# Performance work log

Measured on AMD Instinct MI355X. Metric: run time of the kernel, lower is better.

The kernel has to match this reference:

```python
import jax, jax.numpy as jnp
import numpy as np
from jax import lax


def setup_inputs() -> dict:
    key = jax.random.key(0)
    k1, k2, k3 = jax.random.split(key, 3)
    T, C, H, W = 8, 1024, 64, 64
    features = jax.random.normal(k1, (T, C, H, W), dtype=jnp.float32)
    # Single shared depthwise kernel ([Conv3d]*input_dim shares one module/weight)
    dw_weight = jax.random.normal(k2, (1, 1, 3, 3, 3), dtype=jnp.float32)
    # Pointwise 1x1x1 conv weight [out_c, in_c, 1, 1, 1]
    pw_weight = jax.random.normal(k3, (1024, 1024, 1, 1, 1), dtype=jnp.float32) * 0.03
    return {"features": features, "dw_weight": dw_weight, "pw_weight": pw_weight}


def reference(features, dw_weight, pw_weight):
    T, C, H, W = features.shape
    # torch: expand to [1,T,C,H,W] then torch.reshape to [1,C,T,H,W]
    # (a raw row-major reshape, NOT a transpose) -- replicate exactly.
    x = features.reshape(1, C, T, H, W)
    # Depthwise temporal conv: every channel uses the SAME [1,1,3,3,3] kernel
    # (the torch list is the same Conv3d object repeated). Express as one
    # grouped conv with the kernel tiled over channels.
    w_dw = jnp.tile(dw_weight, (C, 1, 1, 1, 1))  # [C,1,3,3,3]
    y = lax.conv_general_dilated(
        x, w_dw,
        window_strides=(1, 1, 1),
        padding=((1, 1), (1, 1), (1, 1)),
        feature_group_count=C,
        dimension_numbers=("NCDHW", "OIDHW", "NCDHW"),
    )  # [1,C,T,H,W]
    # Pointwise 1x1x1 conv: [C,C] channel-mixing GEMM per voxel.
    z = jnp.einsum("oc,bcthw->bothw", pw_weight[:, :, 0, 0, 0], y)
    # torch: reshape back [1,C,T,H,W] -> [1,T,C,H,W], then squeeze batch dim.
    return z.reshape(1, T, C, H, W)[0]
```

## Files before the change

kernel.cpp:

```cpp
#include <hip/hip_runtime.h>
#include <hip/hip_bf16.h>
#include <stdint.h>

typedef __attribute__((ext_vector_type(8))) short s8v;
typedef __attribute__((ext_vector_type(4))) float f4v;

#define T_TOT 8
#define NSP 32768
#define K_TOT 1024
#define M_TOT 1024

__device__ __forceinline__ unsigned short f2bf(float f) {
  unsigned int u = __float_as_uint(f);
  u += 0x7FFF + ((u >> 16) & 1);
  return (unsigned short)(u >> 16);
}

__global__ __launch_bounds__(256) void dw_kernel(const float* __restrict__ X,
                                                 const float* __restrict__ DW,
                                                 unsigned short* __restrict__ Yn,
                                                 const float* __restrict__ Wf,
                                                 unsigned short* __restrict__ Wb) {
  if (blockIdx.x == 4) {
    const int i = (blockIdx.y * 256 + threadIdx.x) * 4;
    float4 v = *(const float4*)&Wf[i];
    ushort4 o;
    o.x = f2bf(v.x); o.y = f2bf(v.y); o.z = f2bf(v.z); o.w = f2bf(v.w);
    *(ushort4*)&Wb[i] = o;
    return;
  }

  __shared__ float xin[8 * 18 * 64];
  const int tid = threadIdx.x;
  const int hb  = blockIdx.x;
  const int c   = blockIdx.y;
  const int h0  = hb * 16;

  float kw[27];
#pragma unroll
  for (int j = 0; j < 27; ++j) kw[j] = DW[j];

  const float* Xc = X + (size_t)c * NSP;

#pragma unroll
  for (int i = 0; i < 9; ++i) {
    const int f  = tid + i * 256;
    const int r  = f >> 4;
    const int wq = (f & 15) * 4;
    const int t  = r / 18;
    const int hr = r - t * 18;
    const int hg = h0 - 1 + hr;
    const int hc = min(max(hg, 0), 63);
    float4 v = *(const float4*)(Xc + (t * 64 + hc) * 64 + wq);
    if (hg != hc) v = (float4){0.f, 0.f, 0.f, 0.f};
    *(float4*)&xin[r * 64 + wq] = v;
  }
  __syncthreads();

  const int w  = tid & 63;
  const int hq = tid >> 6;
  const int wl = (w == 0)  ? w : w - 1;
  const int wr = (w == 63) ? w : w + 1;
  const float* bC = &xin[(hq * 4) * 64 + w];
  const float* bL = &xin[(hq * 4) * 64 + wl];
  const float* bR = &xin[(hq * 4) * 64 + wr];
  unsigned short* Yb = Yn + (size_t)c * NSP + (h0 + hq * 4) * 64 + w;

  float a0[4], a1[4], a2[4];
#pragma unroll
  for (int j = 0; j < 4; ++j) { a0[j] = 0.f; a1[j] = 0.f; a2[j] = 0.f; }

#pragma unroll
  for (int tp = 0; tp < 8; ++tp) {
    float v[6][3];
#pragma unroll
    for (int rr = 0; rr < 6; ++rr) {
      const int off = (tp * 18 + rr) * 64;
      float xc = bC[off];
      float xl = bL[off];
      float xr = bR[off];
      if (w == 0)  xl = 0.f;
      if (w == 63) xr = 0.f;
      v[rr][0] = xl; v[rr][1] = xc; v[rr][2] = xr;
    }
#pragma unroll
    for (int j = 0; j < 4; ++j)
#pragma unroll
      for (int kh = 0; kh < 3; ++kh)
#pragma unroll
        for (int kd = 0; kd < 3; ++kd) {
          const float xv = v[j + kh][kd];
          if (tp >= 1) a0[j] += kw[(2 * 3 + kh) * 3 + kd] * xv;
          a1[j] += kw[(1 * 3 + kh) * 3 + kd] * xv;
          if (tp <= 6) a2[j] += kw[(0 * 3 + kh) * 3 + kd] * xv;
        }
    if (tp >= 1) {
      unsigned short* yp = Yb + (size_t)(tp - 1) * 4096;
#pragma unroll
      for (int j = 0; j < 4; ++j) yp[j * 64] = f2bf(a0[j]);
    }
#pragma unroll
    for (int j = 0; j < 4; ++j) { a0[j] = a1[j]; a1[j] = a2[j]; a2[j] = 0.f; }
  }
  {
    unsigned short* yp = Yb + (size_t)7 * 4096;
#pragma unroll
    for (int j = 0; j < 4; ++j) yp[j * 64] = f2bf(a0[j]);
  }
}

__global__ __launch_bounds__(256) void tr_kernel(const unsigned short* __restrict__ Yn,
                                                 unsigned short* __restrict__ Yt) {
  __shared__ unsigned short tb[64][68];
  const int tid = threadIdx.x;
  const int n0  = blockIdx.x * 64;
  const int c0  = blockIdx.y * 64;

#pragma unroll
  for (int i = 0; i < 2; ++i) {
    const int cl = (tid >> 3) + i * 32;
    const int n8 = (tid & 7) * 8;
    const uint4 v = *(const uint4*)(Yn + (size_t)(c0 + cl) * NSP + n0 + n8);
    uint2 lo; lo.x = v.x; lo.y = v.y;
    uint2 hi; hi.x = v.z; hi.y = v.w;
    *(uint2*)&tb[cl][n8]     = lo;
    *(uint2*)&tb[cl][n8 + 4] = hi;
  }
  __syncthreads();

  const int nl = tid >> 2;
  const int cq = tid & 3;
#pragma unroll
  for (int i = 0; i < 2; ++i) {
    const int c8 = cq * 8 + i * 32;
    unsigned int p[4];
#pragma unroll
    for (int j = 0; j < 4; ++j) {
      const unsigned int a = tb[c8 + 2 * j][nl];
      const unsigned int b = tb[c8 + 2 * j + 1][nl];
      p[j] = a | (b << 16);
    }
    uint4 o; o.x = p[0]; o.y = p[1]; o.z = p[2]; o.w = p[3];
    *(uint4*)(Yt + (size_t)(n0 + nl) * 1024 + c0 + c8) = o;
  }
}

__device__ __forceinline__ void gload_lds16(const void* g, void* lds) {
  __builtin_amdgcn_global_load_lds(
      (const __attribute__((address_space(1))) void*)(uintptr_t)g,
      (__attribute__((address_space(3))) void*)(uintptr_t)lds, 16, 0, 0);
}

__global__ __launch_bounds__(512, 2) void gemm8_kernel(const unsigned short* __restrict__ A,
                                                       const unsigned short* __restrict__ B,
                                                       float* __restrict__ C) {
  __shared__ char smem[131072];
  const int tid  = threadIdx.x;
  const int lane = tid & 63;
  const int wid  = tid >> 6;
  const int wm   = wid >> 2, wn = wid & 3;

  const int wg = (int)blockIdx.x;
  const int lg = (wg & 7) * 64 + (wg >> 3);
  const int bm = lg & 3;
  const int bn = lg >> 2;

  f4v acc[8][4];
#pragma unroll
  for (int i = 0; i < 8; ++i)
#pragma unroll
    for (int j = 0; j < 4; ++j) acc[i][j] = (f4v){0.f, 0.f, 0.f, 0.f};

  const int r  = tid >> 2;
  const int kb = (((tid & 3) ^ ((tid >> 3) & 3)) * 8);
  const unsigned short* ga = A + (size_t)(bm * 256 + r) * K_TOT + kb;
  const unsigned short* gb = B + (size_t)(bn * 256 + r) * K_TOT + kb;
  const int stg = wid * 1024;

#define STAGE_KK(nb, tt, kk)                                                  \
  do {                                                                        \
    const int ko = (tt) * 64 + (kk) * 32;                                     \
    char* ab = smem + (nb) + (kk) * 16384 + stg;                              \
    char* bb = smem + (nb) + 32768 + (kk) * 16384 + stg;                      \
    gload_lds16(ga + ko,                 ab);                                 \
    gload_lds16(ga + 128 * K_TOT + ko,   ab + 8192);                          \
    gload_lds16(gb + ko,                 bb);                                 \
    gload_lds16(gb + 128 * K_TOT + ko,   bb + 8192);                          \
  } while (0)

  const int cph  = ((lane >> 4) ^ ((lane >> 1) & 3)) * 8;
  const int arow = wm * 128 + (lane & 15);
  const int brow = wn * 64  + (lane & 15);

#define PHASE(cu, nx, tt, kk, pf)                                             \
  do {                                                                        \
    const unsigned short* Ac = (const unsigned short*)(smem + (cu));          \
    const unsigned short* Bc = (const unsigned short*)(smem + (cu) + 32768);  \
    s8v av[8], bv[4];                                                         \
    _Pragma("unroll")                                                         \
    for (int nf = 0; nf < 4; ++nf)                                            \
      bv[nf] = *(const s8v*)&Bc[(kk) * 8192 + (brow + nf * 16) * 32 + cph];   \
    _Pragma("unroll")                                                         \
    for (int mf = 0; mf < 8; ++mf)                                            \
      av[mf] = *(const s8v*)&Ac[(kk) * 8192 + (arow + mf * 16) * 32 + cph];   \
    if (pf) STAGE_KK(nx, (tt) + 1, kk);                                       \
    __builtin_amdgcn_s_setprio(1);                                            \
    _Pragma("unroll")                                                         \
    for (int mf = 0; mf < 8; ++mf)                                            \
      _Pragma("unroll")                                                       \
      for (int nf = 0; nf < 4; ++nf)                                          \
        acc[mf][nf] = __builtin_amdgcn_mfma_f32_16x16x32_bf16(                \
            av[mf], bv[nf], acc[mf][nf], 0, 0, 0);                            \
    __builtin_amdgcn_s_setprio(0);                                            \
  } while (0)

  STAGE_KK(0, 0, 0);
  STAGE_KK(0, 0, 1);

  for (int t = 0; t < 15; ++t) {
    const int cu = (t & 1) << 16;
    const int nx = cu ^ 65536;
    asm volatile("s_waitcnt vmcnt(4)" ::: "memory");
    __builtin_amdgcn_s_barrier();
    PHASE(cu, nx, t, 0, true);
    asm volatile("s_waitcnt vmcnt(4)" ::: "memory");
    __builtin_amdgcn_s_barrier();
    PHASE(cu, nx, t, 1, true);
  }
  asm volatile("s_waitcnt vmcnt(0)" ::: "memory");
  __builtin_amdgcn_s_barrier();
  PHASE(65536, 0, 15, 0, false);
  PHASE(65536, 0, 15, 1, false);

#undef PHASE
#undef STAGE_KK

  const int rowq = (lane >> 4) * 4;
  const int colq = lane & 15;
#pragma unroll
  for (int mf = 0; mf < 8; ++mf) {
    const int row0 = bm * 256 + wm * 128 + mf * 16 + rowq;
#pragma unroll
    for (int nf = 0; nf < 4; ++nf) {
      const int col = bn * 256 + wn * 64 + nf * 16 + colq;
      float* cp = C + (size_t)row0 * NSP + col;
#pragma unroll
      for (int j = 0; j < 4; ++j) cp[(size_t)j * NSP] = acc[mf][nf][j];
    }
  }
}

__global__ __launch_bounds__(256) void gemm_nmajor_kernel(const unsigned short* __restrict__ A,
                                                          const unsigned short* __restrict__ B,
                                                          float* __restrict__ C) {
  __shared__ unsigned short As[128][32];
  __shared__ unsigned short Bs[128][40];
  const int tid  = threadIdx.x;
  const int lane = tid & 63;
  const int wv   = tid >> 6;
  const int wr   = wv >> 1, wc = wv & 1;
  const int bn   = blockIdx.x, bm = blockIdx.y;
  const int n0   = bn * 128;

  f4v acc[4][4];
#pragma unroll
  for (int i = 0; i < 4; ++i)
#pragma unroll
    for (int j = 0; j < 4; ++j) acc[i][j] = (f4v){0.f, 0.f, 0.f, 0.f};

  const int r  = tid >> 2;
  const int kb = (tid & 3) * 8;
  const unsigned short* ga0 = A + (size_t)(bm * 128 + r) * K_TOT + kb;
  char* ldsA = (char*)(&As[0][0]) + wv * 1024;
  const int nq4 = (tid >> 3) * 4;
  const int kq4 = (tid & 7) * 4;

  for (int kt = 0; kt < K_TOT; kt += 32) {
    __syncthreads();
    gload_lds16(ga0 + kt,               ldsA);
    gload_lds16(ga0 + 64 * K_TOT + kt,  ldsA + 4096);

    const unsigned short* gB = B + (size_t)(kt + kq4) * NSP + n0 + nq4;
    uint2 L0 = *(const uint2*)(gB);
    uint2 L1 = *(const uint2*)(gB + NSP);
    uint2 L2 = *(const uint2*)(gB + 2 * NSP);
    uint2 L3 = *(const uint2*)(gB + 3 * NSP);
    uint2 W0, W1, W2, W3;
    W0.x = (L0.x & 0xFFFFu) | (L1.x << 16);
    W0.y = (L2.x & 0xFFFFu) | (L3.x << 16);
    W1.x = (L0.x >> 16) | (L1.x & 0xFFFF0000u);
    W1.y = (L2.x >> 16) | (L3.x & 0xFFFF0000u);
    W2.x = (L0.y & 0xFFFFu) | (L1.y << 16);
    W2.y = (L2.y & 0xFFFFu) | (L3.y << 16);
    W3.x = (L0.y >> 16) | (L1.y & 0xFFFF0000u);
    W3.y = (L2.y >> 16) | (L3.y & 0xFFFF0000u);
    *(uint2*)&Bs[nq4 + 0][kq4] = W0;
    *(uint2*)&Bs[nq4 + 1][kq4] = W1;
    *(uint2*)&Bs[nq4 + 2][kq4] = W2;
    *(uint2*)&Bs[nq4 + 3][kq4] = W3;
    __syncthreads();

    s8v a[4], b[4];
#pragma unroll
    for (int mf = 0; mf < 4; ++mf)
      a[mf] = *(const s8v*)&As[wr * 64 + mf * 16 + (lane & 15)][(lane >> 4) * 8];
#pragma unroll
    for (int nf = 0; nf < 4; ++nf)
      b[nf] = *(const s8v*)&Bs[wc * 64 + nf * 16 + (lane & 15)][(lane >> 4) * 8];
#pragma unroll
    for (int mf = 0; mf < 4; ++mf)
#pragma unroll
      for (int nf = 0; nf < 4; ++nf)
        acc[mf][nf] = __builtin_amdgcn_mfma_f32_16x16x32_bf16(a[mf], b[nf], acc[mf][nf], 0, 0, 0);
  }

  const int rowq = (lane >> 4) * 4;
  const int colq = lane & 15;
#pragma unroll
  for (int mf = 0; mf < 4; ++mf) {
    const int row0 = bm * 128 + wr * 64 + mf * 16 + rowq;
#pragma unroll
    for (int nf = 0; nf < 4; ++nf) {
      const int col = n0 + wc * 64 + nf * 16 + colq;
      float* cp = C + (size_t)row0 * NSP + col;
#pragma unroll
      for (int j = 0; j < 4; ++j) cp[(size_t)j * NSP] = acc[mf][nf][j];
    }
  }
}

extern "C" void kernel_launch(void* const* d_in, const int* in_sizes, int n_in,
                              void* d_out, int out_size, void* d_ws, size_t ws_size,
                              hipStream_t stream) {
  const float* feat = (const float*)d_in[0];
  const float* dw   = (const float*)d_in[1];
  const float* pw   = (const float*)d_in[2];
  float* out = (float*)d_out;

  const size_t YBYTES = (size_t)K_TOT * NSP * 2;
  const size_t WBYTES = (size_t)M_TOT * K_TOT * 2;

  if (ws_size >= 2 * YBYTES + WBYTES) {
    unsigned short* Yt = (unsigned short*)d_ws;
    unsigned short* Yn = (unsigned short*)((char*)d_ws + YBYTES);
    unsigned short* Wb = (unsigned short*)((char*)d_ws + 2 * YBYTES);
    dw_kernel<<<dim3(5, 1024), dim3(256), 0, stream>>>(feat, dw, Yn, pw, Wb);
    tr_kernel<<<dim3(512, 16), dim3(256), 0, stream>>>(Yn, Yt);
    gemm8_kernel<<<dim3(512), dim3(512), 0, stream>>>(Wb, Yt, out);
  } else {
    unsigned short* Yn = (unsigned short*)d_ws;
    unsigned short* Wb = Yn + (size_t)K_TOT * NSP;
    dw_kernel<<<dim3(5, 1024), dim3(256), 0, stream>>>(feat, dw, Yn, pw, Wb);
    gemm_nmajor_kernel<<<dim3(256, 8), dim3(256), 0, stream>>>(Wb, Yn, out);
  }
}
```

Baseline: 149.7 us.

## Restructure GEMM main loop into 8-wave ping-pong schedule with split A/B staging

Rewrites the bf16 GEMM main loop to split LDS reads and MFMA work into four half-tile phases per K-step, separated by barriers. The A and B global-to-LDS prefetches are interleaved across those phases with a deeper prefetch of the next two K-steps. The aim is to overlap memory loads and LDS reads with matrix-core compute, in the style of ping-pong scheduling across waves. In exchange it adds many more barriers per iteration and more complicated vmcnt accounting, which risks stalls or races if the counts are off.

New measurement: 154.3 us. +3.1%, slower.

```diff
diff --git a/kernel.cpp b/kernel.cpp
--- a/kernel.cpp
+++ b/kernel.cpp
@@ -177,63 +177,106 @@
   const unsigned short* gb = B + (size_t)(bn * 256 + r) * K_TOT + kb;
   const int stg = wid * 1024;
 
-#define STAGE_KK(nb, tt, kk)                                                  \
+#define STG_A(nb, tt, kk)                                                     \
   do {                                                                        \
     const int ko = (tt) * 64 + (kk) * 32;                                     \
     char* ab = smem + (nb) + (kk) * 16384 + stg;                              \
+    gload_lds16(ga + ko,               ab);                                   \
+    gload_lds16(ga + 128 * K_TOT + ko, ab + 8192);                            \
+  } while (0)
+#define STG_B(nb, tt, kk)                                                     \
+  do {                                                                        \
+    const int ko = (tt) * 64 + (kk) * 32;                                     \
     char* bb = smem + (nb) + 32768 + (kk) * 16384 + stg;                      \
-    gload_lds16(ga + ko,                 ab);                                 \
-    gload_lds16(ga + 128 * K_TOT + ko,   ab + 8192);                          \
-    gload_lds16(gb + ko,                 bb);                                 \
-    gload_lds16(gb + 128 * K_TOT + ko,   bb + 8192);                          \
+    gload_lds16(gb + ko,               bb);                                   \
+    gload_lds16(gb + 128 * K_TOT + ko, bb + 8192);                            \
   } while (0)
 
   const int cph  = ((lane >> 4) ^ ((lane >> 1) & 3)) * 8;
   const int arow = wm * 128 + (lane & 15);
   const int brow = wn * 64  + (lane & 15);
 
-#define PHASE(cu, nx, tt, kk, pf)                                             \
-  do {                                                                        \
-    const unsigned short* Ac = (const unsigned short*)(smem + (cu));          \
+#define RD_B(cu, kk)                                                          \
+  do {                                                                        \
     const unsigned short* Bc = (const unsigned short*)(smem + (cu) + 32768);  \
-    s8v av[8], bv[4];                                                         \
     _Pragma("unroll")                                                         \
     for (int nf = 0; nf < 4; ++nf)                                            \
       bv[nf] = *(const s8v*)&Bc[(kk) * 8192 + (brow + nf * 16) * 32 + cph];   \
+  } while (0)
+#define RD_A(cu, kk, mb)                                                      \
+  do {                                                                        \
+    const unsigned short* Ac = (const unsigned short*)(smem + (cu));          \
     _Pragma("unroll")                                                         \
-    for (int mf = 0; mf < 8; ++mf)                                            \
-      av[mf] = *(const s8v*)&Ac[(kk) * 8192 + (arow + mf * 16) * 32 + cph];   \
-    if (pf) STAGE_KK(nx, (tt) + 1, kk);                                       \
+    for (int i = 0; i < 4; ++i)                                               \
+      av[i] = *(const s8v*)&Ac[(kk) * 8192 + (arow + ((mb) + i) * 16) * 32 + cph]; \
+  } while (0)
+#define MM(mb)                                                                \
+  do {                                                                        \
     __builtin_amdgcn_s_setprio(1);                                            \
     _Pragma("unroll")                                                         \
-    for (int mf = 0; mf < 8; ++mf)                                            \
+    for (int i = 0; i < 4; ++i)                                               \
       _Pragma("unroll")                                                       \
       for (int nf = 0; nf < 4; ++nf)                                          \
-        acc[mf][nf] = __builtin_amdgcn_mfma_f32_16x16x32_bf16(                \
-            av[mf], bv[nf], acc[mf][nf], 0, 0, 0);                            \
+        acc[(mb) + i][nf] = __builtin_amdgcn_mfma_f32_16x16x32_bf16(          \
+            av[i], bv[nf], acc[(mb) + i][nf], 0, 0, 0);                       \
     __builtin_amdgcn_s_setprio(0);                                            \
   } while (0)
-
-  STAGE_KK(0, 0, 0);
-  STAGE_KK(0, 0, 1);
-
-  for (int t = 0; t < 15; ++t) {
+#define BAR() __builtin_amdgcn_s_barrier()
+
+  STG_B(0, 0, 0); STG_A(0, 0, 0); STG_B(0, 0, 1); STG_A(0, 0, 1);
+  STG_B(65536, 1, 0); STG_A(65536, 1, 0); STG_B(65536, 1, 1);
+  asm volatile("s_waitcnt vmcnt(6)" ::: "memory");
+  BAR();
+
+  s8v av[4], bv[4];
+  for (int t = 0; t < 14; ++t) {
     const int cu = (t & 1) << 16;
-    const int nx = cu ^ 65536;
-    asm volatile("s_waitcnt vmcnt(4)" ::: "memory");
-    __builtin_amdgcn_s_barrier();
-    PHASE(cu, nx, t, 0, true);
-    asm volatile("s_waitcnt vmcnt(4)" ::: "memory");
-    __builtin_amdgcn_s_barrier();
-    PHASE(cu, nx, t, 1, true);
-  }
-  asm volatile("s_waitcnt vmcnt(0)" ::: "memory");
-  __builtin_amdgcn_s_barrier();
-  PHASE(65536, 0, 15, 0, false);
-  PHASE(65536, 0, 15, 1, false);
-
-#undef PHASE
-#undef STAGE_KK
+    const int b1 = cu ^ 65536;
+    RD_B(cu, 0); RD_A(cu, 0, 0);
+    STG_A(b1, t + 1, 1);
+    BAR(); MM(0); BAR();
+    RD_A(cu, 0, 4);
+    STG_B(cu, t + 2, 0);
+    BAR(); MM(4); BAR();
+    RD_B(cu, 1); RD_A(cu, 1, 0);
+    STG_A(cu, t + 2, 0);
+    BAR(); MM(0); BAR();
+    RD_A(cu, 1, 4);
+    STG_B(cu, t + 2, 1);
+    asm volatile("s_waitcnt vmcnt(6)" ::: "memory");
+    BAR(); MM(4); BAR();
+  }
+  {
+    const int cu = 0;
+    RD_B(cu, 0); RD_A(cu, 0, 0);
+    STG_A(65536, 15, 1);
+    BAR(); MM(0); BAR();
+    RD_A(cu, 0, 4);
+    BAR(); MM(4); BAR();
+    RD_B(cu, 1); RD_A(cu, 1, 0);
+    BAR(); MM(0); BAR();
+    RD_A(cu, 1, 4);
+    asm volatile("s_waitcnt vmcnt(0)" ::: "memory");
+    BAR(); MM(4); BAR();
+  }
+  {
+    const int cu = 65536;
+    RD_B(cu, 0); RD_A(cu, 0, 0);
+    BAR(); MM(0); BAR();
+    RD_A(cu, 0, 4);
+    BAR(); MM(4); BAR();
+    RD_B(cu, 1); RD_A(cu, 1, 0);
+    BAR(); MM(0); BAR();
+    RD_A(cu, 1, 4);
+    MM(4);
+  }
+
+#undef BAR
+#undef MM
+#undef RD_A
+#undef RD_B
+#undef STG_A
+#undef STG_B
 
   const int rowq = (lane >> 4) * 4;
   const int colq = lane & 15;
```
